# Kernel tuning notes

Measured on AMD Instinct MI355X. Metric: run time of the kernel, lower is better.

## Reference

```python
import jax, jax.numpy as jnp
import numpy as np

B, S, H = 8, 2048, 1024

def setup_inputs() -> dict:
    key = jax.random.key(0)
    ks = jax.random.split(key, 7)
    scale = 1.0 / np.sqrt(H)
    return {
        "x": jax.random.normal(ks[0], (B, S, H), dtype=jnp.float32),
        "Wq": jax.random.uniform(ks[1], (H, H), jnp.float32, -scale, scale),
        "bq": jax.random.uniform(ks[2], (H,), jnp.float32, -scale, scale),
        "Wk": jax.random.uniform(ks[3], (H, H), jnp.float32, -scale, scale),
        "bk": jax.random.uniform(ks[4], (H,), jnp.float32, -scale, scale),
        "Wv": jax.random.uniform(ks[5], (H, H), jnp.float32, -scale, scale),
        "bv": jax.random.uniform(ks[6], (H,), jnp.float32, -scale, scale),
    }

def reference(x, Wq, bq, Wk, bk, Wv, bv):
    # nn.Linear: x @ W.T + b  (dropout_rate=0.0 -> identity)
    q = jnp.einsum("bsh,oh->bso", x, Wq) + bq
    k = jnp.einsum("bsh,oh->bso", x, Wk) + bk
    v = jnp.einsum("bsh,oh->bso", x, Wv) + bv
    # NOTE: original module applies NO 1/sqrt(d) scaling
    scores = jnp.einsum("bqh,bkh->bqk", q, k)  # [B,S,S]
    probs = jax.nn.softmax(scores, axis=-1)
    context = jnp.einsum("bqk,bkh->bqh", probs, v)  # [B,S,H]
    return context
```

## Files before the change

kernel.cpp:

```cpp
#include <hip/hip_runtime.h>
#include <stdint.h>

typedef unsigned short UST;
typedef __attribute__((ext_vector_type(8))) short    bf16x8;
typedef __attribute__((ext_vector_type(4))) float    f32x4;
typedef __attribute__((ext_vector_type(4))) float    float4_t;
typedef __attribute__((ext_vector_type(4))) UST      ushort4_t;
typedef __attribute__((ext_vector_type(8))) UST      ushort8_t;

__device__ __forceinline__ UST f2bf(float f) {
    union { float f; uint32_t u; } c; c.f = f;
    uint32_t u = c.u;
    u = (u + 0x7FFFu + ((u >> 16) & 1u)) >> 16;
    return (UST)u;
}
__device__ __forceinline__ float bf2f(UST h) {
    union { uint32_t u; float f; } c; c.u = ((uint32_t)h) << 16;
    return c.f;
}

__device__ __forceinline__ void async_copy16(const void* g, void* l) {
    __builtin_amdgcn_global_load_lds(
        (const __attribute__((address_space(1))) uint32_t*)g,
        (__attribute__((address_space(3))) uint32_t*)l, 16, 0, 0);
}

__device__ __forceinline__ void xcd_remap(int& bx, int& by, int& bz) {
    const int gx = (int)gridDim.x, gy = (int)gridDim.y, gz = (int)gridDim.z;
    const int nwg = gx * gy * gz;
    if (nwg & 7) return;
    int flat = ((int)blockIdx.z * gy + (int)blockIdx.y) * gx + (int)blockIdx.x;
    const int q = nwg >> 3;
    int s = (flat & 7) * q + (flat >> 3);
    bx = s % gx; s /= gx;
    by = s % gy;
    bz = s / gy;
}

__global__ void split_kernel(const float* __restrict__ in, UST* __restrict__ hi,
                             UST* __restrict__ lo, int n4) {
    int i = blockIdx.x * blockDim.x + threadIdx.x;
    int stride = gridDim.x * blockDim.x;
    for (; i < n4; i += stride) {
        float4_t v = *(const float4_t*)(in + (size_t)i * 4);
        ushort4_t h, l;
#pragma unroll
        for (int j = 0; j < 4; j++) {
            float f = v[j];
            UST hh = f2bf(f);
            h[j] = hh;
            l[j] = f2bf(f - bf2f(hh));
        }
        *(ushort4_t*)(hi + (size_t)i * 4) = h;
        *(ushort4_t*)(lo + (size_t)i * 4) = l;
    }
}

__global__ void cvt_hi_kernel(const float* __restrict__ in, UST* __restrict__ hi, int n4) {
    int i = blockIdx.x * blockDim.x + threadIdx.x;
    int stride = gridDim.x * blockDim.x;
    for (; i < n4; i += stride) {
        float4_t v = *(const float4_t*)(in + (size_t)i * 4);
        ushort4_t h;
#pragma unroll
        for (int j = 0; j < 4; j++) h[j] = f2bf(v[j]);
        *(ushort4_t*)(hi + (size_t)i * 4) = h;
    }
}

template <int TERMS, int IN_FP32, int OUT_MODE, bool HAS_BIAS>
__global__ __launch_bounds__(256, 2)
void gemm_bt(const void* __restrict__ Aptr, const UST* __restrict__ Al,
             const void* __restrict__ Bptr, const UST* __restrict__ Bl,
             const float* __restrict__ bias,
             void* __restrict__ C0, void* __restrict__ C1,
             int K, int ldc,
             long long sA, long long sB, long long sC) {
    __shared__ UST lds[(TERMS == 3 || OUT_MODE == 2) ? 16384 : 8192];
    UST* tAh = lds;
    UST* tBh = lds + 4096;
    UST* tAl = lds + 8192;
    UST* tBl = lds + 12288;

    int bx = (int)blockIdx.x, by = (int)blockIdx.y, bz = (int)blockIdx.z;
    xcd_remap(bx, by, bz);
    const int brow = by * 128;
    const int bcol = bx * 128;

    const int t = threadIdx.x;
    const int wave = t >> 6, lane = t & 63;
    const int wr = (wave >> 1) * 64, wc = (wave & 1) * 64;
    const int lr = lane & 15, lg = lane >> 4;

    const int srow = t >> 2;
    const int slot = ((t & 3) ^ ((srow >> 1) & 3));
    const int scol_sw = slot * 8;
    const int scol_lin = (t & 3) * 8;

    int offA[4], offB[4];
#pragma unroll
    for (int m = 0; m < 4; m++) {
        int r = wr + m * 16 + lr;
        offA[m] = r * 32 + ((lg ^ ((r >> 1) & 3)) << 3);
    }
#pragma unroll
    for (int n = 0; n < 4; n++) {
        int r = wc + n * 16 + lr;
        offB[n] = r * 32 + ((lg ^ ((r >> 1) & 3)) << 3);
    }

    f32x4 acc[4][4];
#pragma unroll
    for (int m = 0; m < 4; m++)
#pragma unroll
        for (int n = 0; n < 4; n++) acc[m][n] = (f32x4){0.f, 0.f, 0.f, 0.f};

    const UST* Ah = (const UST*)Aptr + (IN_FP32 ? 0 : (long long)bz * sA);
    const UST* Bh = (const UST*)Bptr + (IN_FP32 ? 0 : (long long)bz * sB);
    const float* Af = (const float*)Aptr + (long long)bz * sA;
    const float* Bf = (const float*)Bptr + (long long)bz * sB;
    if constexpr (!IN_FP32) {
        if constexpr (TERMS == 3) {
            Al += (long long)bz * sA;
            Bl += (long long)bz * sB;
        }
    }

    for (int k0 = 0; k0 < K; k0 += 32) {
        if constexpr (IN_FP32) {
#pragma unroll
            for (int h = 0; h < 2; h++) {
                const float* gA = Af + (size_t)(brow + srow + h * 64) * K + k0 + scol_lin;
                float4_t v0 = *(const float4_t*)gA;
                float4_t v1 = *(const float4_t*)(gA + 4);
                ushort4_t h0, h1, l0, l1;
#pragma unroll
                for (int j = 0; j < 4; j++) {
                    h0[j] = f2bf(v0[j]); h1[j] = f2bf(v1[j]);
                    if (TERMS == 3) {
                        l0[j] = f2bf(v0[j] - bf2f(h0[j]));
                        l1[j] = f2bf(v1[j] - bf2f(h1[j]));
                    }
                }
                UST* d = tAh + h * 2048 + srow * 32 + scol_sw;
                *(ushort4_t*)d = h0;
                *(ushort4_t*)(d + 4) = h1;
                if (TERMS == 3) {
                    UST* dl = tAl + h * 2048 + srow * 32 + scol_sw;
                    *(ushort4_t*)dl = l0;
                    *(ushort4_t*)(dl + 4) = l1;
                }
            }
#pragma unroll
            for (int h = 0; h < 2; h++) {
                const float* gB = Bf + (size_t)(bcol + srow + h * 64) * K + k0 + scol_lin;
                float4_t v0 = *(const float4_t*)gB;
                float4_t v1 = *(const float4_t*)(gB + 4);
                ushort4_t h0, h1, l0, l1;
#pragma unroll
                for (int j = 0; j < 4; j++) {
                    h0[j] = f2bf(v0[j]); h1[j] = f2bf(v1[j]);
                    if (TERMS == 3) {
                        l0[j] = f2bf(v0[j] - bf2f(h0[j]));
                        l1[j] = f2bf(v1[j] - bf2f(h1[j]));
                    }
                }
                UST* d = tBh + h * 2048 + srow * 32 + scol_sw;
                *(ushort4_t*)d = h0;
                *(ushort4_t*)(d + 4) = h1;
                if (TERMS == 3) {
                    UST* dl = tBl + h * 2048 + srow * 32 + scol_sw;
                    *(ushort4_t*)dl = l0;
                    *(ushort4_t*)(dl + 4) = l1;
                }
            }
        } else {
            const UST* gA = Ah + (size_t)(brow + srow) * (size_t)K + k0 + scol_sw;
            async_copy16(gA, tAh + t * 8);
            async_copy16(gA + (size_t)64 * K, tAh + 2048 + t * 8);
            const UST* gB = Bh + (size_t)(bcol + srow) * (size_t)K + k0 + scol_sw;
            async_copy16(gB, tBh + t * 8);
            async_copy16(gB + (size_t)64 * K, tBh + 2048 + t * 8);
            if constexpr (TERMS == 3) {
                const UST* gAl = Al + (size_t)(brow + srow) * (size_t)K + k0 + scol_sw;
                async_copy16(gAl, tAl + t * 8);
                async_copy16(gAl + (size_t)64 * K, tAl + 2048 + t * 8);
                const UST* gBl = Bl + (size_t)(bcol + srow) * (size_t)K + k0 + scol_sw;
                async_copy16(gBl, tBl + t * 8);
                async_copy16(gBl + (size_t)64 * K, tBl + 2048 + t * 8);
            }
        }
        __syncthreads();

        bf16x8 ah[4], bh[4];
#pragma unroll
        for (int m = 0; m < 4; m++) ah[m] = *(const bf16x8*)(tAh + offA[m]);
#pragma unroll
        for (int n = 0; n < 4; n++) bh[n] = *(const bf16x8*)(tBh + offB[n]);

        if constexpr (TERMS == 3) {
            bf16x8 al[4], bl[4];
#pragma unroll
            for (int m = 0; m < 4; m++) al[m] = *(const bf16x8*)(tAl + offA[m]);
#pragma unroll
            for (int n = 0; n < 4; n++) bl[n] = *(const bf16x8*)(tBl + offB[n]);
#pragma unroll
            for (int m = 0; m < 4; m++)
#pragma unroll
                for (int n = 0; n < 4; n++) {
                    acc[m][n] = __builtin_amdgcn_mfma_f32_16x16x32_bf16(ah[m], bh[n], acc[m][n], 0, 0, 0);
                    acc[m][n] = __builtin_amdgcn_mfma_f32_16x16x32_bf16(ah[m], bl[n], acc[m][n], 0, 0, 0);
                    acc[m][n] = __builtin_amdgcn_mfma_f32_16x16x32_bf16(al[m], bh[n], acc[m][n], 0, 0, 0);
                }
        } else {
#pragma unroll
            for (int m = 0; m < 4; m++)
#pragma unroll
                for (int n = 0; n < 4; n++)
                    acc[m][n] = __builtin_amdgcn_mfma_f32_16x16x32_bf16(ah[m], bh[n], acc[m][n], 0, 0, 0);
        }
        __syncthreads();
    }

    float bvv[4];
#pragma unroll
    for (int n = 0; n < 4; n++)
        bvv[n] = HAS_BIAS ? bias[bcol + wc + n * 16 + lr] : 0.0f;

    if constexpr (OUT_MODE == 2) {
#pragma unroll
        for (int m = 0; m < 4; m++) {
            const int r0 = wr + m * 16 + lg * 4;
#pragma unroll
            for (int n = 0; n < 4; n++) {
                const int c = wc + n * 16 + lr;
                ushort4_t pk;
#pragma unroll
                for (int j = 0; j < 4; j++) pk[j] = f2bf(acc[m][n][j] + bvv[n]);
                *(ushort4_t*)(lds + c * 128 + r0) = pk;
            }
        }
        __syncthreads();
        UST* V = (UST*)C0 + (long long)bz * sC;
        const int hl = t >> 1, soff = (t & 1) * 64;
        const UST* src = lds + hl * 128 + soff;
        UST* dst = V + (size_t)(bcol + hl) * ldc + brow + soff;
#pragma unroll
        for (int i = 0; i < 8; i++)
            *(ushort8_t*)(dst + i * 8) = *(const ushort8_t*)(src + i * 8);
        return;
    }

#pragma unroll
    for (int m = 0; m < 4; m++) {
        const int row0 = brow + wr + m * 16 + lg * 4;
#pragma unroll
        for (int n = 0; n < 4; n++) {
            const int col = bcol + wc + n * 16 + lr;
            if constexpr (OUT_MODE == 0) {
                float* C = (float*)C0 + (long long)bz * sC;
#pragma unroll
                for (int j = 0; j < 4; j++)
                    C[(size_t)(row0 + j) * ldc + col] = acc[m][n][j] + bvv[n];
            } else if constexpr (OUT_MODE == 1) {
                UST* Hh = (UST*)C0 + (long long)bz * sC;
                UST* Ll = (UST*)C1 + (long long)bz * sC;
#pragma unroll
                for (int j = 0; j < 4; j++) {
                    float v = acc[m][n][j] + bvv[n];
                    UST h = f2bf(v);
                    Hh[(size_t)(row0 + j) * ldc + col] = h;
                    Ll[(size_t)(row0 + j) * ldc + col] = f2bf(v - bf2f(h));
                }
            }
        }
    }
}

__global__ __launch_bounds__(256)
void softmax_bf16(const float* __restrict__ S, UST* __restrict__ P) {
    const size_t row = blockIdx.x;
    const float* s = S + row * 2048;
    const int t = threadIdx.x;
    const int wave = t >> 6, lane = t & 63;

    float4_t v0 = *(const float4_t*)(s + t * 8);
    float4_t v1 = *(const float4_t*)(s + t * 8 + 4);
    float vv[8];
#pragma unroll
    for (int j = 0; j < 4; j++) { vv[j] = v0[j]; vv[4 + j] = v1[j]; }

    float m = vv[0];
#pragma unroll
    for (int j = 1; j < 8; j++) m = fmaxf(m, vv[j]);
#pragma unroll
    for (int off = 32; off; off >>= 1) m = fmaxf(m, __shfl_xor(m, off));

    __shared__ float red[16];
    if (lane == 0) red[wave] = m;
    __syncthreads();
    m = fmaxf(fmaxf(red[0], red[1]), fmaxf(red[2], red[3]));

    float e[8];
    float sum = 0.f;
#pragma unroll
    for (int j = 0; j < 8; j++) { e[j] = __expf(vv[j] - m); sum += e[j]; }
#pragma unroll
    for (int off = 32; off; off >>= 1) sum += __shfl_xor(sum, off);
    if (lane == 0) red[8 + wave] = sum;
    __syncthreads();
    sum = red[8] + red[9] + red[10] + red[11];

    float inv = 1.0f / sum;
    ushort8_t pk;
#pragma unroll
    for (int j = 0; j < 8; j++) pk[j] = f2bf(e[j] * inv);
    *(ushort8_t*)(P + row * 2048 + t * 8) = pk;
}

extern "C" void kernel_launch(void* const* d_in, const int* in_sizes, int n_in,
                              void* d_out, int out_size, void* d_ws, size_t ws_size,
                              hipStream_t stream) {
    (void)in_sizes; (void)n_in; (void)out_size;
    const float* x  = (const float*)d_in[0];
    const float* Wq = (const float*)d_in[1];
    const float* bq = (const float*)d_in[2];
    const float* Wk = (const float*)d_in[3];
    const float* bk = (const float*)d_in[4];
    const float* Wv = (const float*)d_in[5];
    const float* bv = (const float*)d_in[6];
    float* out = (float*)d_out;

    const int B = 8, S = 2048, H = 1024;
    const size_t BSH = (size_t)B * S * H;
    const long long sXH = (long long)S * H;

    char* p = (char*)d_ws;
    UST* qh = (UST*)p; p += BSH * 2;
    UST* ql = (UST*)p; p += BSH * 2;
    UST* kh = (UST*)p; p += BSH * 2;
    UST* kl = (UST*)p; p += BSH * 2;
    UST* vt = (UST*)p; p += BSH * 2;

    const size_t fixed = (size_t)(p - (char*)d_ws);
    const size_t perB = (size_t)S * S * 6;
    const size_t avail = ws_size > fixed ? ws_size - fixed : 0;

    const size_t HH = (size_t)H * H;
    const size_t splitBytes = BSH * 2 * 2 + HH * 2 * 5;

    dim3 blk(256);
    dim3 gproj(H / 128, S / 128, B);

    if (avail >= splitBytes) {
        char* q = p;
        UST* xh  = (UST*)q; q += BSH * 2;
        UST* xl  = (UST*)q; q += BSH * 2;
        UST* wqh = (UST*)q; q += HH * 2;
        UST* wql = (UST*)q; q += HH * 2;
        UST* wkh = (UST*)q; q += HH * 2;
        UST* wkl = (UST*)q; q += HH * 2;
        UST* wvh = (UST*)q; q += HH * 2;

        split_kernel<<<2048, blk, 0, stream>>>(x, xh, xl, (int)(BSH / 4));
        split_kernel<<<256, blk, 0, stream>>>(Wq, wqh, wql, (int)(HH / 4));
        split_kernel<<<256, blk, 0, stream>>>(Wk, wkh, wkl, (int)(HH / 4));
        cvt_hi_kernel<<<256, blk, 0, stream>>>(Wv, wvh, (int)(HH / 4));

        gemm_bt<3, 0, 1, true><<<gproj, blk, 0, stream>>>(xh, xl, wqh, wql, bq, qh, ql, H, H, sXH, 0, sXH);
        gemm_bt<3, 0, 1, true><<<gproj, blk, 0, stream>>>(xh, xl, wkh, wkl, bk, kh, kl, H, H, sXH, 0, sXH);
        gemm_bt<1, 0, 2, true><<<gproj, blk, 0, stream>>>(xh, nullptr, wvh, nullptr, bv, vt, nullptr, H, S, sXH, 0, (long long)H * S);

        int g = (int)(avail / perB);
        if (g > 8) g = 8;
        if (g < 1) g = 1;
        while (8 % g) g--;
        float* scores = (float*)p;
        UST* probs = (UST*)(p + (size_t)g * S * S * 4);

        for (int b0 = 0; b0 < B; b0 += g) {
            dim3 gsc(S / 128, S / 128, g);
            gemm_bt<3, 0, 0, false><<<gsc, blk, 0, stream>>>(
                qh + (size_t)b0 * S * H, ql + (size_t)b0 * S * H,
                kh + (size_t)b0 * S * H, kl + (size_t)b0 * S * H, nullptr,
                scores, nullptr, H, S, sXH, sXH, (long long)S * S);

            softmax_bf16<<<g * S, blk, 0, stream>>>(scores, probs);

            dim3 gpv(H / 128, S / 128, g);
            gemm_bt<1, 0, 0, false><<<gpv, blk, 0, stream>>>(
                probs, nullptr, vt + (size_t)b0 * H * S, nullptr, nullptr,
                out + (size_t)b0 * S * H, nullptr, S, H,
                (long long)S * S, (long long)H * S, sXH);
        }
    } else {
        gemm_bt<3, 1, 1, true><<<gproj, blk, 0, stream>>>(x, nullptr, Wq, nullptr, bq, qh, ql, H, H, sXH, 0, sXH);
        gemm_bt<3, 1, 1, true><<<gproj, blk, 0, stream>>>(x, nullptr, Wk, nullptr, bk, kh, kl, H, H, sXH, 0, sXH);
        gemm_bt<1, 1, 2, true><<<gproj, blk, 0, stream>>>(x, nullptr, Wv, nullptr, bv, vt, nullptr, H, S, sXH, 0, (long long)H * S);

        int rows = (int)(avail / ((size_t)S * 6 * 128)) * 128;
        if (rows < 128) rows = 128;
        if (rows > S) rows = S;
        float* scores = (float*)p;
        UST* probs = (UST*)(p + (size_t)rows * S * 4);

        for (int b = 0; b < B; b++) {
            for (int r0 = 0; r0 < S; r0 += rows) {
                int rc = S - r0 < rows ? S - r0 : rows;
                dim3 gsc(S / 128, rc / 128, 1);
                gemm_bt<3, 0, 0, false><<<gsc, blk, 0, stream>>>(
                    qh + (size_t)b * S * H + (size_t)r0 * H,
                    ql + (size_t)b * S * H + (size_t)r0 * H,
                    kh + (size_t)b * S * H, kl + (size_t)b * S * H, nullptr,
                    scores, nullptr, H, S, 0, 0, 0);

                softmax_bf16<<<rc, blk, 0, stream>>>(scores, probs);

                dim3 gpv(H / 128, rc / 128, 1);
                gemm_bt<1, 0, 0, false><<<gpv, blk, 0, stream>>>(
                    probs, nullptr, vt + (size_t)b * H * S, nullptr, nullptr,
                    out + (size_t)b * S * H + (size_t)r0 * H, nullptr, S, H,
                    0, 0, 0);
            }
        }
    }
}
```

Before: 659.4 us.

## Double-buffer LDS tiles for bf16 GEMM path with async prefetch

For the bf16-input GEMM path, the LDS is split into two buffers and the next K-tile is prefetched with async global-to-LDS copies while MFMAs run on the current tile. One of the two barriers per iteration is removed. The intent is to hide global load latency behind matrix compute. LDS use doubles for that path (up to 64KB for the 3-term variant), which may lower occupancy. The async copies are issued without an explicit wait before the barrier, so correctness relies on the barrier waiting for outstanding loads.

```diff
diff --git a/kernel.cpp b/kernel.cpp
--- a/kernel.cpp
+++ b/kernel.cpp
@@ -76,11 +76,10 @@
              void* __restrict__ C0, void* __restrict__ C1,
              int K, int ldc,
              long long sA, long long sB, long long sC) {
-    __shared__ UST lds[(TERMS == 3 || OUT_MODE == 2) ? 16384 : 8192];
-    UST* tAh = lds;
-    UST* tBh = lds + 4096;
-    UST* tAl = lds + 8192;
-    UST* tBl = lds + 12288;
+    constexpr int HALF = (TERMS == 3) ? 16384 : 8192;
+    constexpr int LREQ = IN_FP32 ? 16384 : 2 * HALF;
+    constexpr int LTOT = LREQ > 16384 ? LREQ : 16384;
+    __shared__ UST lds[LTOT];
 
     int bx = (int)blockIdx.x, by = (int)blockIdx.y, bz = (int)blockIdx.z;
     xcd_remap(bx, by, bz);
@@ -126,8 +125,67 @@
         }
     }
 
-    for (int k0 = 0; k0 < K; k0 += 32) {
-        if constexpr (IN_FP32) {
+    if constexpr (!IN_FP32) {
+        auto stage = [&](UST* dst, int k0) {
+            const UST* gA = Ah + (size_t)(brow + srow) * (size_t)K + k0 + scol_sw;
+            async_copy16(gA, dst + t * 8);
+            async_copy16(gA + (size_t)64 * K, dst + 2048 + t * 8);
+            const UST* gB = Bh + (size_t)(bcol + srow) * (size_t)K + k0 + scol_sw;
+            async_copy16(gB, dst + 4096 + t * 8);
+            async_copy16(gB + (size_t)64 * K, dst + 6144 + t * 8);
+            if constexpr (TERMS == 3) {
+                const UST* gAl = Al + (size_t)(brow + srow) * (size_t)K + k0 + scol_sw;
+                async_copy16(gAl, dst + 8192 + t * 8);
+                async_copy16(gAl + (size_t)64 * K, dst + 10240 + t * 8);
+                const UST* gBl = Bl + (size_t)(bcol + srow) * (size_t)K + k0 + scol_sw;
+                async_copy16(gBl, dst + 12288 + t * 8);
+                async_copy16(gBl + (size_t)64 * K, dst + 14336 + t * 8);
+            }
+        };
+
+        stage(lds, 0);
+        __syncthreads();
+        int cur = 0;
+        for (int k0 = 0; k0 < K; k0 += 32) {
+            UST* buf = lds + cur * HALF;
+            if (k0 + 32 < K) stage(lds + (cur ^ 1) * HALF, k0 + 32);
+
+            bf16x8 ah[4], bh[4];
+#pragma unroll
+            for (int m = 0; m < 4; m++) ah[m] = *(const bf16x8*)(buf + offA[m]);
+#pragma unroll
+            for (int n = 0; n < 4; n++) bh[n] = *(const bf16x8*)(buf + 4096 + offB[n]);
+
+            if constexpr (TERMS == 3) {
+                bf16x8 al[4], bl[4];
+#pragma unroll
+                for (int m = 0; m < 4; m++) al[m] = *(const bf16x8*)(buf + 8192 + offA[m]);
+#pragma unroll
+                for (int n = 0; n < 4; n++) bl[n] = *(const bf16x8*)(buf + 12288 + offB[n]);
+#pragma unroll
+                for (int m = 0; m < 4; m++)
+#pragma unroll
+                    for (int n = 0; n < 4; n++) {
+                        acc[m][n] = __builtin_amdgcn_mfma_f32_16x16x32_bf16(ah[m], bh[n], acc[m][n], 0, 0, 0);
+                        acc[m][n] = __builtin_amdgcn_mfma_f32_16x16x32_bf16(ah[m], bl[n], acc[m][n], 0, 0, 0);
+                        acc[m][n] = __builtin_amdgcn_mfma_f32_16x16x32_bf16(al[m], bh[n], acc[m][n], 0, 0, 0);
+                    }
+            } else {
+#pragma unroll
+                for (int m = 0; m < 4; m++)
+#pragma unroll
+                    for (int n = 0; n < 4; n++)
+                        acc[m][n] = __builtin_amdgcn_mfma_f32_16x16x32_bf16(ah[m], bh[n], acc[m][n], 0, 0, 0);
+            }
+            __syncthreads();
+            cur ^= 1;
+        }
+    } else {
+        UST* tAh = lds;
+        UST* tBh = lds + 4096;
+        UST* tAl = lds + 8192;
+        UST* tBl = lds + 12288;
+        for (int k0 = 0; k0 < K; k0 += 32) {
 #pragma unroll
             for (int h = 0; h < 2; h++) {
                 const float* gA = Af + (size_t)(brow + srow + h * 64) * K + k0 + scol_lin;
@@ -174,52 +232,37 @@
                     *(ushort4_t*)(dl + 4) = l1;
                 }
             }
-        } else {
-            const UST* gA = Ah + (size_t)(brow + srow) * (size_t)K + k0 + scol_sw;
-            async_copy16(gA, tAh + t * 8);
-            async_copy16(gA + (size_t)64 * K, tAh + 2048 + t * 8);
-            const UST* gB = Bh + (size_t)(bcol + srow) * (size_t)K + k0 + scol_sw;
-            async_copy16(gB, tBh + t * 8);
-            async_copy16(gB + (size_t)64 * K, tBh + 2048 + t * 8);
+            __syncthreads();
+
+            bf16x8 ah[4], bh[4];
+#pragma unroll
+            for (int m = 0; m < 4; m++) ah[m] = *(const bf16x8*)(tAh + offA[m]);
+#pragma unroll
+            for (int n = 0; n < 4; n++) bh[n] = *(const bf16x8*)(tBh + offB[n]);
+
             if constexpr (TERMS == 3) {
-                const UST* gAl = Al + (size_t)(brow + srow) * (size_t)K + k0 + scol_sw;
-                async_copy16(gAl, tAl + t * 8);
-                async_copy16(gAl + (size_t)64 * K, tAl + 2048 + t * 8);
-                const UST* gBl = Bl + (size_t)(bcol + srow) * (size_t)K + k0 + scol_sw;
-                async_copy16(gBl, tBl + t * 8);
-                async_copy16(gBl + (size_t)64 * K, tBl + 2048 + t * 8);
-            }
-        }
-        __syncthreads();
-
-        bf16x8 ah[4], bh[4];
-#pragma unroll
-        for (int m = 0; m < 4; m++) ah[m] = *(const bf16x8*)(tAh + offA[m]);
-#pragma unroll
-        for (int n = 0; n < 4; n++) bh[n] = *(const bf16x8*)(tBh + offB[n]);
-
-        if constexpr (TERMS == 3) {
-            bf16x8 al[4], bl[4];
-#pragma unroll
-            for (int m = 0; m < 4; m++) al[m] = *(const bf16x8*)(tAl + offA[m]);
-#pragma unroll
-            for (int n = 0; n < 4; n++) bl[n] = *(const bf16x8*)(tBl + offB[n]);
-#pragma unroll
-            for (int m = 0; m < 4; m++)
-#pragma unroll
-                for (int n = 0; n < 4; n++) {
-                    acc[m][n] = __builtin_amdgcn_mfma_f32_16x16x32_bf16(ah[m], bh[n], acc[m][n], 0, 0, 0);
-                    acc[m][n] = __builtin_amdgcn_mfma_f32_16x16x32_bf16(ah[m], bl[n], acc[m][n], 0, 0, 0);
-                    acc[m][n] = __builtin_amdgcn_mfma_f32_16x16x32_bf16(al[m], bh[n], acc[m][n], 0, 0, 0);
-                }
-        } else {
-#pragma unroll
-            for (int m = 0; m < 4; m++)
-#pragma unroll
-                for (int n = 0; n < 4; n++)
-                    acc[m][n] = __builtin_amdgcn_mfma_f32_16x16x32_bf16(ah[m], bh[n], acc[m][n], 0, 0, 0);
-        }
-        __syncthreads();
+                bf16x8 al[4], bl[4];
+#pragma unroll
+                for (int m = 0; m < 4; m++) al[m] = *(const bf16x8*)(tAl + offA[m]);
+#pragma unroll
+                for (int n = 0; n < 4; n++) bl[n] = *(const bf16x8*)(tBl + offB[n]);
+#pragma unroll
+                for (int m = 0; m < 4; m++)
+#pragma unroll
+                    for (int n = 0; n < 4; n++) {
+                        acc[m][n] = __builtin_amdgcn_mfma_f32_16x16x32_bf16(ah[m], bh[n], acc[m][n], 0, 0, 0);
+                        acc[m][n] = __builtin_amdgcn_mfma_f32_16x16x32_bf16(ah[m], bl[n], acc[m][n], 0, 0, 0);
+                        acc[m][n] = __builtin_amdgcn_mfma_f32_16x16x32_bf16(al[m], bh[n], acc[m][n], 0, 0, 0);
+                    }
+            } else {
+#pragma unroll
+                for (int m = 0; m < 4; m++)
+#pragma unroll
+                    for (int n = 0; n < 4; n++)
+                        acc[m][n] = __builtin_amdgcn_mfma_f32_16x16x32_bf16(ah[m], bh[n], acc[m][n], 0, 0, 0);
+            }
+            __syncthreads();
+        }
     }
 
     float bvv[4];
```

Result: faster. 600.2 us (-9.0%).

## Pipeline GEMM with triple-buffered async LDS loads and phase-serialized split terms

Applied to the files above, without the earlier changes.

Rewrites the bf16 GEMM to stage tiles into a three-slot LDS ring with async global-to-LDS copies issued two iterations ahead. Waits use explicit vmcnt counts instead of a full sync after every k-step. The three-term split precision product becomes three sequential K passes (hi*hi, lo*hi, hi*lo) over the same pipeline, so only two fragments sit in registers at a time. Occupancy is raised to 3 blocks per CU, the fp32-input fallback is removed, and the split kernels now always run. This trades larger LDS use and more loop iterations for overlap of memory loads with MFMA work.

```diff
diff --git a/kernel.cpp b/kernel.cpp
--- a/kernel.cpp
+++ b/kernel.cpp
@@ -68,19 +68,18 @@
     }
 }
 
-template <int TERMS, int IN_FP32, int OUT_MODE, bool HAS_BIAS>
-__global__ __launch_bounds__(256, 2)
-void gemm_bt(const void* __restrict__ Aptr, const UST* __restrict__ Al,
-             const void* __restrict__ Bptr, const UST* __restrict__ Bl,
+template <int NPHASE, int OUT_MODE, bool HAS_BIAS>
+__global__ __launch_bounds__(256, 3)
+void gemm_bt(const UST* __restrict__ A0, const UST* __restrict__ A1,
+             const UST* __restrict__ A2,
+             const UST* __restrict__ B0, const UST* __restrict__ B1,
+             const UST* __restrict__ B2,
              const float* __restrict__ bias,
              void* __restrict__ C0, void* __restrict__ C1,
              int K, int ldc,
              long long sA, long long sB, long long sC) {
-    __shared__ UST lds[(TERMS == 3 || OUT_MODE == 2) ? 16384 : 8192];
-    UST* tAh = lds;
-    UST* tBh = lds + 4096;
-    UST* tAl = lds + 8192;
-    UST* tBl = lds + 12288;
+    constexpr int HALF = 8192;
+    __shared__ UST lds[3 * HALF];
 
     int bx = (int)blockIdx.x, by = (int)blockIdx.y, bz = (int)blockIdx.z;
     xcd_remap(bx, by, bz);
@@ -93,9 +92,8 @@
     const int lr = lane & 15, lg = lane >> 4;
 
     const int srow = t >> 2;
-    const int slot = ((t & 3) ^ ((srow >> 1) & 3));
-    const int scol_sw = slot * 8;
-    const int scol_lin = (t & 3) * 8;
+    const int slotc = ((t & 3) ^ ((srow >> 1) & 3));
+    const int scol_sw = slotc * 8;
 
     int offA[4], offB[4];
 #pragma unroll
@@ -115,111 +113,64 @@
 #pragma unroll
         for (int n = 0; n < 4; n++) acc[m][n] = (f32x4){0.f, 0.f, 0.f, 0.f};
 
-    const UST* Ah = (const UST*)Aptr + (IN_FP32 ? 0 : (long long)bz * sA);
-    const UST* Bh = (const UST*)Bptr + (IN_FP32 ? 0 : (long long)bz * sB);
-    const float* Af = (const float*)Aptr + (long long)bz * sA;
-    const float* Bf = (const float*)Bptr + (long long)bz * sB;
-    if constexpr (!IN_FP32) {
-        if constexpr (TERMS == 3) {
-            Al += (long long)bz * sA;
-            Bl += (long long)bz * sB;
-        }
-    }
-
-    for (int k0 = 0; k0 < K; k0 += 32) {
-        if constexpr (IN_FP32) {
-#pragma unroll
-            for (int h = 0; h < 2; h++) {
-                const float* gA = Af + (size_t)(brow + srow + h * 64) * K + k0 + scol_lin;
-                float4_t v0 = *(const float4_t*)gA;
-                float4_t v1 = *(const float4_t*)(gA + 4);
-                ushort4_t h0, h1, l0, l1;
-#pragma unroll
-                for (int j = 0; j < 4; j++) {
-                    h0[j] = f2bf(v0[j]); h1[j] = f2bf(v1[j]);
-                    if (TERMS == 3) {
-                        l0[j] = f2bf(v0[j] - bf2f(h0[j]));
-                        l1[j] = f2bf(v1[j] - bf2f(h1[j]));
-                    }
-                }
-                UST* d = tAh + h * 2048 + srow * 32 + scol_sw;
-                *(ushort4_t*)d = h0;
-                *(ushort4_t*)(d + 4) = h1;
-                if (TERMS == 3) {
-                    UST* dl = tAl + h * 2048 + srow * 32 + scol_sw;
-                    *(ushort4_t*)dl = l0;
-                    *(ushort4_t*)(dl + 4) = l1;
-                }
-            }
-#pragma unroll
-            for (int h = 0; h < 2; h++) {
-                const float* gB = Bf + (size_t)(bcol + srow + h * 64) * K + k0 + scol_lin;
-                float4_t v0 = *(const float4_t*)gB;
-                float4_t v1 = *(const float4_t*)(gB + 4);
-                ushort4_t h0, h1, l0, l1;
-#pragma unroll
-                for (int j = 0; j < 4; j++) {
-                    h0[j] = f2bf(v0[j]); h1[j] = f2bf(v1[j]);
-                    if (TERMS == 3) {
-                        l0[j] = f2bf(v0[j] - bf2f(h0[j]));
-                        l1[j] = f2bf(v1[j] - bf2f(h1[j]));
-                    }
-                }
-                UST* d = tBh + h * 2048 + srow * 32 + scol_sw;
-                *(ushort4_t*)d = h0;
-                *(ushort4_t*)(d + 4) = h1;
-                if (TERMS == 3) {
-                    UST* dl = tBl + h * 2048 + srow * 32 + scol_sw;
-                    *(ushort4_t*)dl = l0;
-                    *(ushort4_t*)(dl + 4) = l1;
-                }
-            }
+    const UST* a0 = A0 + (long long)bz * sA;
+    const UST* b0 = B0 + (long long)bz * sB;
+    const UST* a1 = (NPHASE > 1) ? A1 + (long long)bz * sA : nullptr;
+    const UST* b1 = (NPHASE > 1) ? B1 + (long long)bz * sB : nullptr;
+    const UST* a2 = (NPHASE > 2) ? A2 + (long long)bz * sA : nullptr;
+    const UST* b2 = (NPHASE > 2) ? B2 + (long long)bz * sB : nullptr;
+
+    int sph = 0, sk = 0;
+    auto stage = [&](int slot) {
+        const UST* pA = (NPHASE > 1 && sph == 1) ? a1
+                      : (NPHASE > 2 && sph == 2) ? a2 : a0;
+        const UST* pB = (NPHASE > 1 && sph == 1) ? b1
+                      : (NPHASE > 2 && sph == 2) ? b2 : b0;
+        UST* dst = lds + slot * HALF;
+        const UST* gA = pA + (size_t)(brow + srow) * (size_t)K + sk + scol_sw;
+        async_copy16(gA, dst + t * 8);
+        async_copy16(gA + (size_t)64 * K, dst + 2048 + t * 8);
+        const UST* gB = pB + (size_t)(bcol + srow) * (size_t)K + sk + scol_sw;
+        async_copy16(gB, dst + 4096 + t * 8);
+        async_copy16(gB + (size_t)64 * K, dst + 6144 + t * 8);
+        sk += 32;
+        if (sk == K) { sk = 0; ++sph; }
+    };
+
+    const int ntotal = NPHASE * (K / 32);
+    stage(0);
+    if (ntotal > 1) stage(1);
+    int slot = 0;
+    for (int it = 0; it < ntotal; ++it) {
+        __builtin_amdgcn_s_barrier();
+        const int rem = ntotal - 1 - it;
+        if (rem >= 2) {
+            int s2 = slot + 2; if (s2 >= 3) s2 -= 3;
+            stage(s2);
+            asm volatile("s_waitcnt vmcnt(8)" ::: "memory");
+        } else if (rem == 1) {
+            asm volatile("s_waitcnt vmcnt(4)" ::: "memory");
         } else {
-            const UST* gA = Ah + (size_t)(brow + srow) * (size_t)K + k0 + scol_sw;
-            async_copy16(gA, tAh + t * 8);
-            async_copy16(gA + (size_t)64 * K, tAh + 2048 + t * 8);
-            const UST* gB = Bh + (size_t)(bcol + srow) * (size_t)K + k0 + scol_sw;
-            async_copy16(gB, tBh + t * 8);
-            async_copy16(gB + (size_t)64 * K, tBh + 2048 + t * 8);
-            if constexpr (TERMS == 3) {
-                const UST* gAl = Al + (size_t)(brow + srow) * (size_t)K + k0 + scol_sw;
-                async_copy16(gAl, tAl + t * 8);
-                async_copy16(gAl + (size_t)64 * K, tAl + 2048 + t * 8);
-                const UST* gBl = Bl + (size_t)(bcol + srow) * (size_t)K + k0 + scol_sw;
-                async_copy16(gBl, tBl + t * 8);
-                async_copy16(gBl + (size_t)64 * K, tBl + 2048 + t * 8);
-            }
-        }
-        __syncthreads();
-
+            asm volatile("s_waitcnt vmcnt(0)" ::: "memory");
+        }
+        __builtin_amdgcn_sched_barrier(0);
+        __builtin_amdgcn_s_barrier();
+
+        UST* buf = lds + slot * HALF;
         bf16x8 ah[4], bh[4];
 #pragma unroll
-        for (int m = 0; m < 4; m++) ah[m] = *(const bf16x8*)(tAh + offA[m]);
-#pragma unroll
-        for (int n = 0; n < 4; n++) bh[n] = *(const bf16x8*)(tBh + offB[n]);
-
-        if constexpr (TERMS == 3) {
-            bf16x8 al[4], bl[4];
-#pragma unroll
-            for (int m = 0; m < 4; m++) al[m] = *(const bf16x8*)(tAl + offA[m]);
-#pragma unroll
-            for (int n = 0; n < 4; n++) bl[n] = *(const bf16x8*)(tBl + offB[n]);
-#pragma unroll
-            for (int m = 0; m < 4; m++)
-#pragma unroll
-                for (int n = 0; n < 4; n++) {
-                    acc[m][n] = __builtin_amdgcn_mfma_f32_16x16x32_bf16(ah[m], bh[n], acc[m][n], 0, 0, 0);
-                    acc[m][n] = __builtin_amdgcn_mfma_f32_16x16x32_bf16(ah[m], bl[n], acc[m][n], 0, 0, 0);
-                    acc[m][n] = __builtin_amdgcn_mfma_f32_16x16x32_bf16(al[m], bh[n], acc[m][n], 0, 0, 0);
-                }
-        } else {
-#pragma unroll
-            for (int m = 0; m < 4; m++)
-#pragma unroll
-                for (int n = 0; n < 4; n++)
-                    acc[m][n] = __builtin_amdgcn_mfma_f32_16x16x32_bf16(ah[m], bh[n], acc[m][n], 0, 0, 0);
-        }
-        __syncthreads();
+        for (int m = 0; m < 4; m++) ah[m] = *(const bf16x8*)(buf + offA[m]);
+#pragma unroll
+        for (int n = 0; n < 4; n++) bh[n] = *(const bf16x8*)(buf + 4096 + offB[n]);
+
+        __builtin_amdgcn_s_setprio(1);
+#pragma unroll
+        for (int m = 0; m < 4; m++)
+#pragma unroll
+            for (int n = 0; n < 4; n++)
+                acc[m][n] = __builtin_amdgcn_mfma_f32_16x16x32_bf16(ah[m], bh[n], acc[m][n], 0, 0, 0);
+        __builtin_amdgcn_s_setprio(0);
+        ++slot; if (slot == 3) slot = 0;
     }
 
     float bvv[4];
@@ -228,6 +179,7 @@
         bvv[n] = HAS_BIAS ? bias[bcol + wc + n * 16 + lr] : 0.0f;
 
     if constexpr (OUT_MODE == 2) {
+        __syncthreads();
 #pragma unroll
         for (int m = 0; m < 4; m++) {
             const int r0 = wr + m * 16 + lg * 4;
@@ -347,57 +299,58 @@
     const size_t avail = ws_size > fixed ? ws_size - fixed : 0;
 
     const size_t HH = (size_t)H * H;
-    const size_t splitBytes = BSH * 2 * 2 + HH * 2 * 5;
+
+    char* q = p;
+    UST* xh  = (UST*)q; q += BSH * 2;
+    UST* xl  = (UST*)q; q += BSH * 2;
+    UST* wqh = (UST*)q; q += HH * 2;
+    UST* wql = (UST*)q; q += HH * 2;
+    UST* wkh = (UST*)q; q += HH * 2;
+    UST* wkl = (UST*)q; q += HH * 2;
+    UST* wvh = (UST*)q; q += HH * 2;
 
     dim3 blk(256);
+
+    split_kernel<<<2048, blk, 0, stream>>>(x, xh, xl, (int)(BSH / 4));
+    split_kernel<<<256, blk, 0, stream>>>(Wq, wqh, wql, (int)(HH / 4));
+    split_kernel<<<256, blk, 0, stream>>>(Wk, wkh, wkl, (int)(HH / 4));
+    cvt_hi_kernel<<<256, blk, 0, stream>>>(Wv, wvh, (int)(HH / 4));
+
     dim3 gproj(H / 128, S / 128, B);
-
-    if (avail >= splitBytes) {
-        char* q = p;
-        UST* xh  = (UST*)q; q += BSH * 2;
-        UST* xl  = (UST*)q; q += BSH * 2;
-        UST* wqh = (UST*)q; q += HH * 2;
-        UST* wql = (UST*)q; q += HH * 2;
-        UST* wkh = (UST*)q; q += HH * 2;
-        UST* wkl = (UST*)q; q += HH * 2;
-        UST* wvh = (UST*)q; q += HH * 2;
-
-        split_kernel<<<2048, blk, 0, stream>>>(x, xh, xl, (int)(BSH / 4));
-        split_kernel<<<256, blk, 0, stream>>>(Wq, wqh, wql, (int)(HH / 4));
-        split_kernel<<<256, blk, 0, stream>>>(Wk, wkh, wkl, (int)(HH / 4));
-        cvt_hi_kernel<<<256, blk, 0, stream>>>(Wv, wvh, (int)(HH / 4));
-
-        gemm_bt<3, 0, 1, true><<<gproj, blk, 0, stream>>>(xh, xl, wqh, wql, bq, qh, ql, H, H, sXH, 0, sXH);
-        gemm_bt<3, 0, 1, true><<<gproj, blk, 0, stream>>>(xh, xl, wkh, wkl, bk, kh, kl, H, H, sXH, 0, sXH);
-        gemm_bt<1, 0, 2, true><<<gproj, blk, 0, stream>>>(xh, nullptr, wvh, nullptr, bv, vt, nullptr, H, S, sXH, 0, (long long)H * S);
-
-        int g = (int)(avail / perB);
+    gemm_bt<3, 1, true><<<gproj, blk, 0, stream>>>(
+        xh, xl, xh, wqh, wqh, wql, bq, qh, ql, H, H, sXH, 0, sXH);
+    gemm_bt<3, 1, true><<<gproj, blk, 0, stream>>>(
+        xh, xl, xh, wkh, wkh, wkl, bk, kh, kl, H, H, sXH, 0, sXH);
+    gemm_bt<1, 2, true><<<gproj, blk, 0, stream>>>(
+        xh, nullptr, nullptr, wvh, nullptr, nullptr, bv, vt, nullptr,
+        H, S, sXH, 0, (long long)H * S);
+
+    int g = (int)(avail / perB);
+    if (g >= 1) {
         if (g > 8) g = 8;
-        if (g < 1) g = 1;
         while (8 % g) g--;
         float* scores = (float*)p;
         UST* probs = (UST*)(p + (size_t)g * S * S * 4);
 
         for (int b0 = 0; b0 < B; b0 += g) {
+            const UST* qhb = qh + (size_t)b0 * S * H;
+            const UST* qlb = ql + (size_t)b0 * S * H;
+            const UST* khb = kh + (size_t)b0 * S * H;
+            const UST* klb = kl + (size_t)b0 * S * H;
             dim3 gsc(S / 128, S / 128, g);
-            gemm_bt<3, 0, 0, false><<<gsc, blk, 0, stream>>>(
-                qh + (size_t)b0 * S * H, ql + (size_t)b0 * S * H,
-                kh + (size_t)b0 * S * H, kl + (size_t)b0 * S * H, nullptr,
+            gemm_bt<3, 0, false><<<gsc, blk, 0, stream>>>(
+                qhb, qlb, qhb, khb, khb, klb, nullptr,
                 scores, nullptr, H, S, sXH, sXH, (long long)S * S);
 
             softmax_bf16<<<g * S, blk, 0, stream>>>(scores, probs);
 
             dim3 gpv(H / 128, S / 128, g);
-            gemm_bt<1, 0, 0, false><<<gpv, blk, 0, stream>>>(
-                probs, nullptr, vt + (size_t)b0 * H * S, nullptr, nullptr,
-                out + (size_t)b0 * S * H, nullptr, S, H,
+            gemm_bt<1, 0, false><<<gpv, blk, 0, stream>>>(
+                probs, nullptr, nullptr, vt + (size_t)b0 * H * S, nullptr, nullptr,
+                nullptr, out + (size_t)b0 * S * H, nullptr, S, H,
                 (long long)S * S, (long long)H * S, sXH);
         }
     } else {
-        gemm_bt<3, 1, 1, true><<<gproj, blk, 0, stream>>>(x, nullptr, Wq, nullptr, bq, qh, ql, H, H, sXH, 0, sXH);
-        gemm_bt<3, 1, 1, true><<<gproj, blk, 0, stream>>>(x, nullptr, Wk, nullptr, bk, kh, kl, H, H, sXH, 0, sXH);
-        gemm_bt<1, 1, 2, true><<<gproj, blk, 0, stream>>>(x, nullptr, Wv, nullptr, bv, vt, nullptr, H, S, sXH, 0, (long long)H * S);
-
         int rows = (int)(avail / ((size_t)S * 6 * 128)) * 128;
         if (rows < 128) rows = 128;
         if (rows > S) rows = S;
@@ -407,19 +360,21 @@
         for (int b = 0; b < B; b++) {
             for (int r0 = 0; r0 < S; r0 += rows) {
                 int rc = S - r0 < rows ? S - r0 : rows;
+                const UST* qhb = qh + (size_t)b * S * H + (size_t)r0 * H;
+                const UST* qlb = ql + (size_t)b * S * H + (size_t)r0 * H;
+                const UST* khb = kh + (size_t)b * S * H;
+                const UST* klb = kl + (size_t)b * S * H;
                 dim3 gsc(S / 128, rc / 128, 1);
-                gemm_bt<3, 0, 0, false><<<gsc, blk, 0, stream>>>(
-                    qh + (size_t)b * S * H + (size_t)r0 * H,
-                    ql + (size_t)b * S * H + (size_t)r0 * H,
-                    kh + (size_t)b * S * H, kl + (size_t)b * S * H, nullptr,
+                gemm_bt<3, 0, false><<<gsc, blk, 0, stream>>>(
+                    qhb, qlb, qhb, khb, khb, klb, nullptr,
                     scores, nullptr, H, S, 0, 0, 0);
 
                 softmax_bf16<<<rc, blk, 0, stream>>>(scores, probs);
 
                 dim3 gpv(H / 128, rc / 128, 1);
-                gemm_bt<1, 0, 0, false><<<gpv, blk, 0, stream>>>(
-                    probs, nullptr, vt + (size_t)b * H * S, nullptr, nullptr,
-                    out + (size_t)b * S * H + (size_t)r0 * H, nullptr, S, H,
+                gemm_bt<1, 0, false><<<gpv, blk, 0, stream>>>(
+                    probs, nullptr, nullptr, vt + (size_t)b * H * S, nullptr, nullptr,
+                    nullptr, out + (size_t)b * S * H + (size_t)r0 * H, nullptr, S, H,
                     0, 0, 0);
             }
         }
```

After: 1.319 ms. 100% more time.
